# Kernel optimization log

Hardware: AMD Instinct MI355X
Metric: run time of the kernel (lower is better)

## Reference

```python
import jax, jax.numpy as jnp
import numpy as np

B, T, D_MODEL, HEAD_DIM = 4, 4096, 1024, 2


def setup_inputs() -> dict:
    key = jax.random.key(0)
    kx, kq, kk, kv = jax.random.split(key, 4)
    x = jax.random.normal(kx, (B, T, D_MODEL), dtype=jnp.float32)
    # nn.Linear weights: (out_features, in_features), applied as x @ W.T
    s_qk = 1.0 / np.sqrt(D_MODEL)
    W_Q = jax.random.uniform(kq, (HEAD_DIM, D_MODEL), minval=-s_qk, maxval=s_qk, dtype=jnp.float32)
    W_K = jax.random.uniform(kk, (HEAD_DIM, D_MODEL), minval=-s_qk, maxval=s_qk, dtype=jnp.float32)
    W_V = jax.random.uniform(kv, (D_MODEL, D_MODEL), minval=-s_qk, maxval=s_qk, dtype=jnp.float32)
    # strict upper-triangular True = masked (future positions)
    causal_mask = jnp.triu(jnp.ones((T, T), dtype=bool), k=1)[None, :, :]
    return {"x": x, "W_Q": W_Q, "W_K": W_K, "W_V": W_V, "causal_mask": causal_mask}


def reference(x, W_Q, W_K, W_V, causal_mask):
    # x: (B, T, d_model)
    Q = jnp.einsum('btd,hd->bth', x, W_Q)   # (B, T, head_dim)
    K = jnp.einsum('bsd,hd->bsh', x, W_K)   # (B, S, head_dim)
    V = jnp.einsum('bsd,ed->bse', x, W_V)   # (B, S, d_model)
    scores = jnp.einsum('bth,bsh->bts', Q, K)              # (B, T, S)
    scores = jnp.where(causal_mask, -jnp.inf, scores)
    max_idx = jnp.argmax(scores, axis=-1)                  # (B, T)
    # one-hot scatter + bmm in the original == hard gather of V rows
    out = jnp.take_along_axis(V, max_idx[..., None], axis=1)  # (B, T, d_model)
    return out
```

## Files before the change

### kernel.cpp

```cpp
#include <hip/hip_runtime.h>
#include <math.h>

#define TT 4096
#define DM 1024
#define BB 4
#define BT (BB * TT)
#define SENT  0x7f7f7f7f
#define MAGIC 0x17C3A5E9
#define NBLK 1024


__device__ __forceinline__ float dot4(const float4 a, const float4 b) {
    return a.x * b.x + a.y * b.y + a.z * b.z + a.w * b.w;
}
__device__ __forceinline__ int aload(const int* p) {
    return __hip_atomic_load((int*)p, __ATOMIC_RELAXED, __HIP_MEMORY_SCOPE_AGENT);
}
__device__ __forceinline__ void astore(int* p, int v) {
    __hip_atomic_store(p, v, __ATOMIC_RELAXED, __HIP_MEMORY_SCOPE_AGENT);
}
__device__ __forceinline__ void astore64(unsigned long long* p, unsigned long long v) {
    __hip_atomic_store(p, v, __ATOMIC_RELAXED, __HIP_MEMORY_SCOPE_AGENT);
}
__device__ __forceinline__ unsigned long long packf2(float a, float b) {
    union { float2 f; unsigned long long u; } cv;
    cv.f = make_float2(a, b);
    return cv.u;
}
__device__ __forceinline__ void spin_eq(const int* p, int v) {
    int it = 0;
    while (__hip_atomic_load((int*)p, __ATOMIC_RELAXED, __HIP_MEMORY_SCOPE_AGENT) != v) {
        __builtin_amdgcn_s_sleep(8);
        if (++it > (1 << 21)) break;
    }
}

__global__ __launch_bounds__(256, 4) void mega_kernel(
    const float* __restrict__ x, const float* __restrict__ wq,
    const float* __restrict__ wk, const float* __restrict__ wv,
    unsigned long long* __restrict__ Qu, unsigned long long* __restrict__ Ku,
    int* __restrict__ idx, int* __restrict__ rep, int* __restrict__ rowdone,
    int* __restrict__ chunkdone, int* __restrict__ blkdone,
    int* __restrict__ gen, float* __restrict__ out)
{
    __shared__ union {
        float4 w[4][256];
        float2 ks[TT];
        struct { int n; int g[4095]; } hits;
    } sm;

    const int tid  = threadIdx.x;
    const int bid  = blockIdx.x;
    const int wave = tid >> 6, lane = tid & 63;

    const int expv = MAGIC ^ aload(gen);

    if (bid < 512) {
        sm.w[0][tid] = ((const float4*)(wq))[tid];
        sm.w[1][tid] = ((const float4*)(wq + DM))[tid];
        sm.w[2][tid] = ((const float4*)(wk))[tid];
        sm.w[3][tid] = ((const float4*)(wk + DM))[tid];
        if (tid < 32) {
            const int rg = bid * 32 + tid;
            astore(&rep[rg], SENT);
            astore(&idx[rg], -1);
            astore(&rowdone[rg], 0);
        }
        __syncthreads();

        #pragma unroll
        for (int rr = 0; rr < 8; ++rr) {
            const int row = bid * 32 + wave * 8 + rr;
            const float4* xr = (const float4*)(x + (size_t)row * DM);
            float s0 = 0.f, s1 = 0.f, s2 = 0.f, s3 = 0.f;
            #pragma unroll
            for (int j = 0; j < 4; ++j) {
                const float4 xv = xr[j * 64 + lane];
                s0 += dot4(xv, sm.w[0][j * 64 + lane]);
                s1 += dot4(xv, sm.w[1][j * 64 + lane]);
                s2 += dot4(xv, sm.w[2][j * 64 + lane]);
                s3 += dot4(xv, sm.w[3][j * 64 + lane]);
            }
            #pragma unroll
            for (int off = 32; off > 0; off >>= 1) {
                s0 += __shfl_down(s0, off);
                s1 += __shfl_down(s1, off);
                s2 += __shfl_down(s2, off);
                s3 += __shfl_down(s3, off);
            }
            if (lane == 0) {
                astore64(&Qu[row], packf2(s0, s1));
                astore64(&Ku[row], packf2(s2, s3));
            }
        }
        __syncthreads();
        if (tid == 0) astore(&chunkdone[bid], expv);
    }

    const float* Kf = (const float*)Ku;
    const float* Qf = (const float*)Qu;
    for (int pp = 0; pp < 2; ++pp) {
        const int p = bid * 2 + pp;
        const int b = p >> 9, j = p & 511;
        const int cmax = ((1023 - j) * 4 + 3) >> 5;
        if (tid <= cmax) spin_eq(&chunkdone[b * 128 + tid], expv);
        __syncthreads();

        const int nfill4 = (((1023 - j) * 4 + 4) >> 1);
        const float4* kb4 = (const float4*)(Kf + (size_t)b * TT * 2);
        float4* ks4 = (float4*)sm.ks;
        for (int i = tid; i < nfill4; i += 256) ks4[i] = kb4[i];
        __syncthreads();

        const float4* kp = (const float4*)sm.ks;
        #pragma unroll
        for (int u = 0; u < 2; ++u) {
            const int tg = u ? j : (1023 - j);
            const int t = tg * 4 + wave;
            const float2 q = ((const float2*)Qf)[b * TT + t];

            float best = -INFINITY;
            int bi = 0x7fffffff;
            int pq = lane;
            while (2 * (pq + 64) + 1 <= t) {
                const float4 a = kp[pq];
                const float4 c = kp[pq + 64];
                const float c0 = q.x * a.x + q.y * a.y;
                const float c1 = q.x * a.z + q.y * a.w;
                const float c2 = q.x * c.x + q.y * c.y;
                const float c3 = q.x * c.z + q.y * c.w;
                if (c0 > best) { best = c0; bi = 2 * pq; }
                if (c1 > best) { best = c1; bi = 2 * pq + 1; }
                if (c2 > best) { best = c2; bi = 2 * (pq + 64); }
                if (c3 > best) { best = c3; bi = 2 * (pq + 64) + 1; }
                pq += 128;
            }
            while (2 * pq <= t) {
                const float4 a = kp[pq];
                const float c0 = q.x * a.x + q.y * a.y;
                if (c0 > best) { best = c0; bi = 2 * pq; }
                if (2 * pq + 1 <= t) {
                    const float c1 = q.x * a.z + q.y * a.w;
                    if (c1 > best) { best = c1; bi = 2 * pq + 1; }
                }
                pq += 64;
            }
            #pragma unroll
            for (int off = 32; off > 0; off >>= 1) {
                const float ov = __shfl_down(best, off);
                const int   oi = __shfl_down(bi, off);
                if (ov > best || (ov == best && oi < bi)) { best = ov; bi = oi; }
            }
            if (lane == 0) {
                astore(&idx[b * TT + t], bi);
                atomicMin(&rep[b * TT + bi], t);
            }
        }
        __syncthreads();
    }
    if (tid == 0) astore(&blkdone[bid], expv);

    const int slice = bid >> 4;
    const int usub  = bid & 15;
    const int e0 = slice * 16 + wave * 4;
    float4 w[4][4];
    #pragma unroll
    for (int r = 0; r < 4; ++r) {
        const float4* wr = (const float4*)(wv + (size_t)(e0 + r) * DM);
        #pragma unroll
        for (int jj = 0; jj < 4; ++jj) w[r][jj] = wr[jj * 64 + lane];
    }
    {
        #pragma unroll
        for (int k = 0; k < 4; ++k) spin_eq(&blkdone[tid + 256 * k], expv);
    }
    __syncthreads();
    if (tid == 0) sm.hits.n = 0;
    __syncthreads();
    #pragma unroll
    for (int k = 0; k < 4; ++k) {
        const int m = tid + 256 * k;
        const int g = usub + (m << 4);
        const int s = aload(&idx[g]);
        const int b2 = g >> 12;
        if (aload(&rep[(b2 << 12) + s]) == (g & (TT - 1))) {
            const int pos = atomicAdd(&sm.hits.n, 1);
            sm.hits.g[pos] = g;
        }
    }
    __syncthreads();
    const int nh = sm.hits.n;
    for (int h = 0; h < nh; ++h) {
        const int g  = sm.hits.g[h];
        const int b2 = g >> 12;
        const int s  = aload(&idx[g]);
        const int bs = (b2 << 12) + s;
        const float4* xr = (const float4*)(x + (size_t)bs * DM);
        float4 xv[4];
        #pragma unroll
        for (int jj = 0; jj < 4; ++jj) xv[jj] = xr[jj * 64 + lane];
        float s0 = 0.f, s1 = 0.f, s2 = 0.f, s3 = 0.f;
        #pragma unroll
        for (int jj = 0; jj < 4; ++jj) {
            s0 += dot4(w[0][jj], xv[jj]);
            s1 += dot4(w[1][jj], xv[jj]);
            s2 += dot4(w[2][jj], xv[jj]);
            s3 += dot4(w[3][jj], xv[jj]);
        }
        #pragma unroll
        for (int off = 32; off > 0; off >>= 1) {
            s0 += __shfl_down(s0, off);
            s1 += __shfl_down(s1, off);
            s2 += __shfl_down(s2, off);
            s3 += __shfl_down(s3, off);
        }
        if (lane == 0) {
            unsigned long long* op = (unsigned long long*)(out + (size_t)g * DM + e0);
            astore64(op,     packf2(s0, s1));
            astore64(op + 1, packf2(s2, s3));
        }
        __syncthreads();
        if (tid == 0) atomicAdd(&rowdone[bs], 1);
    }

    for (int r4 = 0; r4 < 4; ++r4) {
        const int g  = bid * 16 + r4 * 4 + wave;
        const int b2 = g >> 12, tl = g & (TT - 1);
        const int s  = aload(&idx[g]);
        const int bs = (b2 << 12) + s;
        const int r  = aload(&rep[bs]);
        if (r == tl) continue;
        int it = 0;
        while (aload(&rowdone[bs]) != 64) {
            __builtin_amdgcn_s_sleep(8);
            if (++it > (1 << 21)) break;
        }
        asm volatile("" ::: "memory");
        const float4* src = (const float4*)(out + ((size_t)(b2 * TT + r)) * DM);
        float4* dst = (float4*)(out + (size_t)g * DM);
        #pragma unroll
        for (int k2 = 0; k2 < 4; ++k2) dst[k2 * 64 + lane] = src[k2 * 64 + lane];
    }

    __syncthreads();
    if (bid == 0 && tid == 0) atomicAdd(gen, 1);
}

extern "C" void kernel_launch(void* const* d_in, const int* in_sizes, int n_in,
                              void* d_out, int out_size, void* d_ws, size_t ws_size,
                              hipStream_t stream) {
    const float* x  = (const float*)d_in[0];
    const float* wq = (const float*)d_in[1];
    const float* wk = (const float*)d_in[2];
    const float* wv = (const float*)d_in[3];
    float* out = (float*)d_out;

    char* ws = (char*)d_ws;
    unsigned long long* Qu = (unsigned long long*)(ws);
    unsigned long long* Ku = (unsigned long long*)(ws + 131072);
    int* idx       = (int*)(ws + 262144);
    int* rep       = (int*)(ws + 327680);
    int* rowdone   = (int*)(ws + 393216);
    int* chunkdone = (int*)(ws + 458752);
    int* blkdone   = (int*)(ws + 460800);
    int* gen       = (int*)(ws + 464896);

    mega_kernel<<<NBLK, 256, 0, stream>>>(x, wq, wk, wv, Qu, Ku,
                                          idx, rep, rowdone,
                                          chunkdone, blkdone, gen, out);
}
```

Before: 238.0 us.

## Split persistent mega-kernel into QK-argmax and V-gather kernels

```diff
diff --git a/kernel.cpp b/kernel.cpp
--- a/kernel.cpp
+++ b/kernel.cpp
@@ -7,7 +7,6 @@
 #define BT (BB * TT)
 #define SENT  0x7f7f7f7f
 #define MAGIC 0x17C3A5E9
-#define NBLK 1024
 
 
 __device__ __forceinline__ float dot4(const float4 a, const float4 b) {
@@ -35,18 +34,16 @@
     }
 }
 
-__global__ __launch_bounds__(256, 4) void mega_kernel(
+__global__ __launch_bounds__(256, 4) void qk_am_kernel(
     const float* __restrict__ x, const float* __restrict__ wq,
-    const float* __restrict__ wk, const float* __restrict__ wv,
+    const float* __restrict__ wk,
     unsigned long long* __restrict__ Qu, unsigned long long* __restrict__ Ku,
     int* __restrict__ idx, int* __restrict__ rep, int* __restrict__ rowdone,
-    int* __restrict__ chunkdone, int* __restrict__ blkdone,
-    int* __restrict__ gen, float* __restrict__ out)
+    int* __restrict__ chunkdone, const int* __restrict__ gen)
 {
     __shared__ union {
         float4 w[4][256];
         float2 ks[TT];
-        struct { int n; int g[4095]; } hits;
     } sm;
 
     const int tid  = threadIdx.x;
@@ -158,7 +155,20 @@
         }
         __syncthreads();
     }
-    if (tid == 0) astore(&blkdone[bid], expv);
+}
+
+__global__ __launch_bounds__(256, 4) void vrow_gather_kernel(
+    const float* __restrict__ x, const float* __restrict__ wv,
+    const int* __restrict__ idx, const int* __restrict__ rep,
+    int* __restrict__ rowdone, int* __restrict__ gen,
+    float* __restrict__ out)
+{
+    __shared__ int hits_n;
+    __shared__ int hits_g[4096];
+
+    const int tid  = threadIdx.x;
+    const int bid  = blockIdx.x;
+    const int wave = tid >> 6, lane = tid & 63;
 
     const int slice = bid >> 4;
     const int usub  = bid & 15;
@@ -170,28 +180,23 @@
         #pragma unroll
         for (int jj = 0; jj < 4; ++jj) w[r][jj] = wr[jj * 64 + lane];
     }
-    {
-        #pragma unroll
-        for (int k = 0; k < 4; ++k) spin_eq(&blkdone[tid + 256 * k], expv);
-    }
-    __syncthreads();
-    if (tid == 0) sm.hits.n = 0;
+    if (tid == 0) hits_n = 0;
     __syncthreads();
     #pragma unroll
     for (int k = 0; k < 4; ++k) {
-        const int m = tid + 256 * k;
-        const int g = usub + (m << 4);
+        const int m4 = tid + 256 * k;
+        const int g = usub + (m4 << 4);
         const int s = aload(&idx[g]);
         const int b2 = g >> 12;
         if (aload(&rep[(b2 << 12) + s]) == (g & (TT - 1))) {
-            const int pos = atomicAdd(&sm.hits.n, 1);
-            sm.hits.g[pos] = g;
+            const int pos = atomicAdd(&hits_n, 1);
+            hits_g[pos] = g;
         }
     }
     __syncthreads();
-    const int nh = sm.hits.n;
+    const int nh = hits_n;
     for (int h = 0; h < nh; ++h) {
-        const int g  = sm.hits.g[h];
+        const int g  = hits_g[h];
         const int b2 = g >> 12;
         const int s  = aload(&idx[g]);
         const int bs = (b2 << 12) + s;
@@ -262,10 +267,10 @@
     int* rep       = (int*)(ws + 327680);
     int* rowdone   = (int*)(ws + 393216);
     int* chunkdone = (int*)(ws + 458752);
-    int* blkdone   = (int*)(ws + 460800);
-    int* gen       = (int*)(ws + 464896);
-
-    mega_kernel<<<NBLK, 256, 0, stream>>>(x, wq, wk, wv, Qu, Ku,
-                                          idx, rep, rowdone,
-                                          chunkdone, blkdone, gen, out);
-}
+    int* gen       = (int*)(ws + 460800);
+
+    qk_am_kernel<<<1024, 256, 0, stream>>>(x, wq, wk, Qu, Ku,
+                                           idx, rep, rowdone, chunkdone, gen);
+    vrow_gather_kernel<<<1024, 256, 0, stream>>>(x, wv, idx, rep,
+                                                 rowdone, gen, out);
+}
```

New measurement: 229.2 us. -3.7%, faster.
